# Kernel optimization log

Hardware: AMD Instinct MI355X
Metric: run time of the kernel (lower is better)

Reference implementation:

```python
import jax, jax.numpy as jnp
import numpy as np
import math

# ---- static config (must match init_kwargs / input_specs) ----
D = 1024
N_HEAD = 16
HEAD_DIM = D // N_HEAD          # 64
HALF = HEAD_DIM // 2            # rope half dim = 32
N_EXP = 8
TOP_K = 2
CAP_FACTOR = 2.0
LN_EPS = 1e-5


def _build_sin_cos(T, half_dim, dtype=jnp.float32):
    pos = jnp.arange(T, dtype=dtype)[:, None]                      # (T,1)
    inv_freq = 1.0 / (10000.0 ** (jnp.arange(0, 2 * half_dim, 2, dtype=dtype) / (2 * half_dim)))
    ang = pos * inv_freq[None, :]                                  # (T, half)
    return jnp.sin(ang), jnp.cos(ang)


def _layernorm(x, g, b):
    mu = jnp.mean(x, axis=-1, keepdims=True)
    var = jnp.mean(jnp.square(x - mu), axis=-1, keepdims=True)
    return (x - mu) * jax.lax.rsqrt(var + LN_EPS) * g + b


def _apply_rope(q, k, sin, cos):
    # q,k: (B,T,H,hd); sin,cos: (T, half)
    s = sin[None, :, None, :]
    c = cos[None, :, None, :]
    q1, q2 = q[..., :HALF], q[..., HALF:]
    k1, k2 = k[..., :HALF], k[..., HALF:]
    qr = jnp.concatenate([q1 * c - q2 * s, q1 * s + q2 * c], axis=-1)
    kr = jnp.concatenate([k1 * c - k2 * s, k1 * s + k2 * c], axis=-1)
    return qr, kr


def _attention(x, Wqkv, Wproj):
    B, T, C = x.shape
    qkv = x @ Wqkv                                                  # (B,T,3C)
    qkv = qkv.reshape(B, T, N_HEAD, 3 * HEAD_DIM)
    q, k, v = jnp.split(qkv, 3, axis=-1)                            # each (B,T,H,hd)
    sin, cos = _build_sin_cos(T, HALF)
    q, k = _apply_rope(q, k, sin, cos)
    scale = 1.0 / math.sqrt(HEAD_DIM)
    att = jnp.einsum('bqhd,bkhd->bhqk', q, k) * scale               # (B,H,T,T)
    causal = jnp.tril(jnp.ones((T, T), dtype=bool))
    att = jnp.where(causal[None, None], att, jnp.finfo(att.dtype).min)
    p = jax.nn.softmax(att, axis=-1)
    o = jnp.einsum('bhqk,bkhd->bqhd', p, v).reshape(B, T, C)
    return o @ Wproj, k, v


def _sparse_moe(flat, Wgate, W1, b1, W2, b2):
    # flat: (N, d). Eval mode: no router noise.
    N, d = flat.shape
    capacity = int(math.ceil(CAP_FACTOR * N / N_EXP))
    logits = flat @ Wgate                                           # (N,E)
    gates = jax.nn.softmax(logits, axis=-1)
    vals, inds = jax.lax.top_k(gates, TOP_K)                        # (N,k)
    flat_inds = inds.reshape(-1)                                    # (N*k,)
    flat_vals = vals.reshape(-1)
    neg = jnp.finfo(flat.dtype).min
    # per-expert assignment scores over all (token, slot) pairs
    scores = jnp.where(flat_inds[None, :] == jnp.arange(N_EXP)[:, None],
                       flat_vals[None, :], neg)                     # (E, N*k)
    top_scores, top_pos = jax.lax.top_k(scores, capacity)           # (E, cap)
    tok_idx = top_pos // TOP_K                                      # (E, cap)
    w = jnp.where(top_scores > neg, top_scores, 0.0)                # dropped slots -> 0 weight
    xe = flat[tok_idx]                                              # gather: (E, cap, d)
    h = jax.nn.gelu(jnp.einsum('ecd,edh->ech', xe, W1) + b1[:, None, :], approximate=False)
    out = jnp.einsum('ech,ehd->ecd', h, W2) + b2[:, None, :]
    out = out * w[..., None]
    final = jnp.zeros_like(flat).at[tok_idx.reshape(-1)].add(out.reshape(-1, d))
    return final


def setup_inputs() -> dict:
    key = jax.random.key(0)
    ks = jax.random.split(key, 10)
    B, T = 2, 2048
    s = 0.02
    return {
        'x': jax.random.normal(ks[0], (B, T, D), dtype=jnp.float32),
        'ln1_g': jnp.ones((D,), jnp.float32),
        'ln1_b': jnp.zeros((D,), jnp.float32),
        'ln2_g': jnp.ones((D,), jnp.float32),
        'ln2_b': jnp.zeros((D,), jnp.float32),
        'Wqkv': jax.random.normal(ks[1], (D, 3 * D), jnp.float32) * s,
        'Wproj': jax.random.normal(ks[2], (D, D), jnp.float32) * s,
        'Wgate': jax.random.normal(ks[3], (D, N_EXP), jnp.float32) * s,
        'W1': jax.random.normal(ks[4], (N_EXP, D, 4 * D), jnp.float32) * s,
        'b1': jnp.zeros((N_EXP, 4 * D), jnp.float32),
        'W2': jax.random.normal(ks[5], (N_EXP, 4 * D, D), jnp.float32) * s,
        'b2': jnp.zeros((N_EXP, D), jnp.float32),
    }


def reference(x, ln1_g, ln1_b, ln2_g, ln2_b, Wqkv, Wproj, Wgate, W1, b1, W2, b2):
    B, T, _ = x.shape
    x_norm = _layernorm(x, ln1_g, ln1_b)
    attn_out, k, v = _attention(x_norm, Wqkv, Wproj)
    x = x + attn_out
    ff_in = _layernorm(x, ln2_g, ln2_b)
    moe_out = _sparse_moe(ff_in.reshape(B * T, D), Wgate, W1, b1, W2, b2)
    x = x + moe_out.reshape(B, T, D)
    aux_loss = jnp.zeros((), x.dtype)  # eval mode
    return x, aux_loss, k, v
```

## Files before the change

kernel.cpp:

```cpp
#include <hip/hip_runtime.h>
#include <hip/hip_bf16.h>
#include <math.h>


#define TT 2048
#define NTOK 4096

typedef __attribute__((ext_vector_type(8))) short bf16x8;
typedef __attribute__((ext_vector_type(4))) float f32x4;
typedef __attribute__((ext_vector_type(16))) float f32x16;

static __device__ __forceinline__ ushort f2bf(float f) {
  union { float f; unsigned u; } v; v.f = f;
  unsigned r = v.u + 0x7FFFu + ((v.u >> 16) & 1u);
  return (ushort)(r >> 16);
}
static __device__ __forceinline__ float bf2f(ushort h) {
  union { unsigned u; float f; } v; v.u = ((unsigned)h) << 16; return v.f;
}
static __device__ __forceinline__ unsigned cvt_pk_bf16(float lo, float hi) {
  unsigned r;
  asm("v_cvt_pk_bf16_f32 %0, %1, %2" : "=v"(r) : "v"(lo), "v"(hi));
  return r;
}
static __device__ __forceinline__ void plane_swap(unsigned& a, unsigned& b) {
  asm("v_permlane32_swap_b32 %0, %1" : "+v"(a), "+v"(b));
}
static __device__ __forceinline__ void gload16(const void* g, void* l) {
  __builtin_amdgcn_global_load_lds(
      (const __attribute__((address_space(1))) void*)g,
      (__attribute__((address_space(3))) void*)l, 16, 0, 0);
}

template<bool WF32>
__global__ __launch_bounds__(256)
void ln_kernel(const float* __restrict__ x, const float* __restrict__ g,
               const float* __restrict__ b, float* __restrict__ out,
               ushort* __restrict__ oh, ushort* __restrict__ ol) {
  int row = blockIdx.x, tid = threadIdx.x;
  const float4* xr = (const float4*)(x + (size_t)row * 1024);
  float4 v = xr[tid];
  float s = v.x + v.y + v.z + v.w;
  #pragma unroll
  for (int off = 1; off < 64; off <<= 1) s += __shfl_xor(s, off);
  __shared__ float red1[4], red2[4];
  if ((tid & 63) == 0) red1[tid >> 6] = s;
  __syncthreads();
  float mu = (red1[0] + red1[1] + red1[2] + red1[3]) * (1.0f / 1024.0f);
  float dx = v.x - mu, dy = v.y - mu, dz = v.z - mu, dw = v.w - mu;
  float ss = dx*dx + dy*dy + dz*dz + dw*dw;
  #pragma unroll
  for (int off = 1; off < 64; off <<= 1) ss += __shfl_xor(ss, off);
  if ((tid & 63) == 0) red2[tid >> 6] = ss;
  __syncthreads();
  float var = (red2[0] + red2[1] + red2[2] + red2[3]) * (1.0f / 1024.0f);
  float inv = 1.0f / sqrtf(var + 1e-5f);
  float4 g4 = ((const float4*)g)[tid];
  float4 b4 = ((const float4*)b)[tid];
  float4 o4;
  o4.x = dx * inv * g4.x + b4.x;
  o4.y = dy * inv * g4.y + b4.y;
  o4.z = dz * inv * g4.z + b4.z;
  o4.w = dw * inv * g4.w + b4.w;
  if constexpr (WF32)
    ((float4*)(out + (size_t)row * 1024))[tid] = o4;
  size_t base = (size_t)row * 1024 + tid * 4;
  ushort h0 = f2bf(o4.x), h1 = f2bf(o4.y), h2 = f2bf(o4.z), h3 = f2bf(o4.w);
  ushort4 hh = {h0, h1, h2, h3};
  *(ushort4*)(oh + base) = hh;
  ushort4 ll = {f2bf(o4.x - bf2f(h0)), f2bf(o4.y - bf2f(h1)),
                f2bf(o4.z - bf2f(h2)), f2bf(o4.w - bf2f(h3))};
  *(ushort4*)(ol + base) = ll;
}

__global__ void sincos_kernel(float* __restrict__ st, float* __restrict__ ct) {
  int t = blockIdx.x, j = threadIdx.x;
  double invf = pow(10000.0, -((double)(2 * j)) / 64.0);
  double ang = (double)t * invf;
  st[t * 32 + j] = (float)sin(ang);
  ct[t * 32 + j] = (float)cos(ang);
}

__global__ __launch_bounds__(256)
void rope_kernel(float* __restrict__ qkv, const float* __restrict__ st,
                 const float* __restrict__ ct, float* __restrict__ kout,
                 float* __restrict__ vout, ushort* __restrict__ Kh,
                 ushort* __restrict__ Kl) {
  int row = blockIdx.x;
  int t = row & (TT - 1);
  int b = row >> 11;
  int tid = threadIdx.x;
  float* base = qkv + (size_t)row * 3072;
  #pragma unroll
  for (int l = 0; l < 2; ++l) {
    int idx = l * 256 + tid;
    int h = idx >> 5, j = idx & 31;
    float s = st[t * 32 + j], c = ct[t * 32 + j];
    float* qp = base + h * 192;
    float q1 = qp[j], q2 = qp[j + 32];
    qp[j]      = q1 * c - q2 * s;
    qp[j + 32] = q1 * s + q2 * c;
    float k1 = qp[64 + j], k2 = qp[96 + j];
    float kr1 = k1 * c - k2 * s, kr2 = k1 * s + k2 * c;
    qp[64 + j] = kr1; qp[96 + j] = kr2;
    kout[(size_t)row * 1024 + h * 64 + j]      = kr1;
    kout[(size_t)row * 1024 + h * 64 + 32 + j] = kr2;
    size_t kb = ((size_t)(b * 16 + h) * TT + t) * 64;
    ushort h1 = f2bf(kr1);
    Kh[kb + j] = h1; Kl[kb + j] = f2bf(kr1 - bf2f(h1));
    ushort h2 = f2bf(kr2);
    Kh[kb + 32 + j] = h2; Kl[kb + 32 + j] = f2bf(kr2 - bf2f(h2));
  }
  #pragma unroll
  for (int l = 0; l < 4; ++l) {
    int f = l * 256 + tid;
    int h = f >> 6, d = f & 63;
    vout[(size_t)row * 1024 + f] = base[h * 192 + 128 + d];
  }
}

__global__ __launch_bounds__(256)
void vtprep_kernel(const float* __restrict__ vout, ushort* __restrict__ Vth,
                   ushort* __restrict__ Vtl) {
  __shared__ float tile[64][65];
  int t0 = blockIdx.x * 64, h = blockIdx.y, b = blockIdx.z;
  int tid = threadIdx.x;
  #pragma unroll
  for (int l = 0; l < 4; ++l) {
    int idx = l * 256 + tid;
    int r = idx >> 4, c4 = (idx & 15) * 4;
    *(float4*)&tile[r][c4] = *(const float4*)&vout[((size_t)(b * TT + t0 + r)) * 1024 + h * 64 + c4];
  }
  __syncthreads();
  int d = tid >> 2, ts = (tid & 3) * 16;
  union { bf16x8 v; ushort u[8]; } H0, H1, L0, L1;
  #pragma unroll
  for (int i = 0; i < 8; ++i) {
    float v0 = tile[ts + i][d];
    ushort hb0 = f2bf(v0);
    H0.u[i] = hb0; L0.u[i] = f2bf(v0 - bf2f(hb0));
    float v1 = tile[ts + 8 + i][d];
    ushort hb1 = f2bf(v1);
    H1.u[i] = hb1; L1.u[i] = f2bf(v1 - bf2f(hb1));
  }
  size_t basep = ((size_t)(b * 16 + h) * 64 + d) * TT + t0 + ts;
  *(bf16x8*)(Vth + basep) = H0.v;  *(bf16x8*)(Vth + basep + 8) = H1.v;
  *(bf16x8*)(Vtl + basep) = L0.v;  *(bf16x8*)(Vtl + basep + 8) = L1.v;
}

__global__ __launch_bounds__(256)
void flash6_kernel(const float* __restrict__ qkv, const ushort* __restrict__ Kh,
                   const ushort* __restrict__ Kl, const ushort* __restrict__ Vth,
                   const ushort* __restrict__ Vtl, float* __restrict__ Opart,
                   float* __restrict__ Mpart, float* __restrict__ Lpart) {
  int lin = blockIdx.x;
  int xcd = lin & 7, s = lin >> 3;
  int bh = xcd + 8 * (s / 40);
  int j = 39 - (s % 40);
  int qt, kc;
  if (j < 4)       { qt = j;                    kc = 0; }
  else if (j < 12) { qt = 4 + ((j - 4) >> 1);   kc = (j - 4) & 1; }
  else if (j < 24) { qt = 8 + (j - 12) / 3;     kc = (j - 12) % 3; }
  else             { qt = 12 + ((j - 24) >> 2); kc = (j - 24) & 3; }
  int slot = bh * 40 + j;
  int h = bh & 15, b = bh >> 4;
  int tid = threadIdx.x;
  int w = tid >> 6, lane = tid & 63;
  int q = lane & 31, LH = lane >> 5;
  size_t bT = (size_t)b * TT;
  int qglob0 = qt * 128 + w * 32;
  int qg = qglob0 + q;
  bf16x8 qH[4], qL[4];
  {
    const float* qp = qkv + (bT + qg) * 3072 + h * 192 + LH * 8;
    #pragma unroll
    for (int dblk = 0; dblk < 4; ++dblk) {
      float4 f0 = *(const float4*)(qp + dblk * 16);
      float4 f1 = *(const float4*)(qp + dblk * 16 + 4);
      float vals[8] = {f0.x, f0.y, f0.z, f0.w, f1.x, f1.y, f1.z, f1.w};
      union { bf16x8 v; ushort u[8]; } H, L;
      #pragma unroll
      for (int e = 0; e < 8; ++e) {
        ushort hb = f2bf(vals[e]);
        H.u[e] = hb; L.u[e] = f2bf(vals[e] - bf2f(hb));
      }
      qH[dblk] = H.v; qL[dblk] = L.v;
    }
  }
  const ushort* Kbh = Kh + (size_t)bh * TT * 64;
  const ushort* Kbl = Kl + (size_t)bh * TT * 64;
  const ushort* Vbh = Vth + (size_t)bh * 64 * TT;
  const ushort* Vbl = Vtl + (size_t)bh * 64 * TT;
  f32x16 accO0 = {}, accO1 = {};
  float m = -3.402823466e38f, lsum = 0.0f;
  int kvlo = kc * 512;
  int kvhi = min(kc * 512 + 512, qglob0 + 32);

  for (int kv0 = kvlo; kv0 < kvhi; kv0 += 32) {
    const ushort* kbh = Kbh + (size_t)(kv0 + q) * 64 + LH * 8;
    const ushort* kbl = Kbl + (size_t)(kv0 + q) * 64 + LH * 8;
    bf16x8 kAH[4], kAL[4];
    #pragma unroll
    for (int dblk = 0; dblk < 4; ++dblk) {
      kAH[dblk] = *(const bf16x8*)(kbh + dblk * 16);
      kAL[dblk] = *(const bf16x8*)(kbl + dblk * 16);
    }
    f32x16 sa = {}, sb = {};
    sa = __builtin_amdgcn_mfma_f32_32x32x16_bf16(kAH[0], qH[0], sa, 0, 0, 0);
    sb = __builtin_amdgcn_mfma_f32_32x32x16_bf16(kAH[2], qH[2], sb, 0, 0, 0);
    sa = __builtin_amdgcn_mfma_f32_32x32x16_bf16(kAH[1], qH[1], sa, 0, 0, 0);
    sb = __builtin_amdgcn_mfma_f32_32x32x16_bf16(kAH[3], qH[3], sb, 0, 0, 0);
    sa = __builtin_amdgcn_mfma_f32_32x32x16_bf16(kAH[0], qL[0], sa, 0, 0, 0);
    sb = __builtin_amdgcn_mfma_f32_32x32x16_bf16(kAH[2], qL[2], sb, 0, 0, 0);
    sa = __builtin_amdgcn_mfma_f32_32x32x16_bf16(kAH[1], qL[1], sa, 0, 0, 0);
    sb = __builtin_amdgcn_mfma_f32_32x32x16_bf16(kAH[3], qL[3], sb, 0, 0, 0);
    sa = __builtin_amdgcn_mfma_f32_32x32x16_bf16(kAL[0], qH[0], sa, 0, 0, 0);
    sb = __builtin_amdgcn_mfma_f32_32x32x16_bf16(kAL[2], qH[2], sb, 0, 0, 0);
    sa = __builtin_amdgcn_mfma_f32_32x32x16_bf16(kAL[1], qH[1], sa, 0, 0, 0);
    sb = __builtin_amdgcn_mfma_f32_32x32x16_bf16(kAL[3], qH[3], sb, 0, 0, 0);
    bf16x8 vAH[2][2], vAL[2][2];
    #pragma unroll
    for (int dblk = 0; dblk < 2; ++dblk)
      #pragma unroll
      for (int s2 = 0; s2 < 2; ++s2) {
        size_t ad = (size_t)(dblk * 32 + q) * TT + kv0 + s2 * 16 + LH * 8;
        vAH[dblk][s2] = *(const bf16x8*)(Vbh + ad);
        vAL[dblk][s2] = *(const bf16x8*)(Vbl + ad);
      }
    float p[16];
    float pmax = -3.402823466e38f;
    if (kv0 + 31 > qglob0) {
      #pragma unroll
      for (int r = 0; r < 16; ++r) {
        int kvg = kv0 + (r & 3) + 8 * (r >> 2) + 4 * LH;
        float sv = (kvg <= qg) ? (sa[r] + sb[r]) * 0.125f : -3.402823466e38f;
        p[r] = sv; pmax = fmaxf(pmax, sv);
      }
    } else {
      #pragma unroll
      for (int r = 0; r < 16; ++r) {
        float sv = (sa[r] + sb[r]) * 0.125f;
        p[r] = sv; pmax = fmaxf(pmax, sv);
      }
    }
    pmax = fmaxf(pmax, __shfl_xor(pmax, 32));
    float mnew = fmaxf(m, pmax);
    float fsc = __expf(m - mnew);
    float psum = 0.0f;
    #pragma unroll
    for (int r = 0; r < 16; ++r) { p[r] = __expf(p[r] - mnew); psum += p[r]; }
    psum += __shfl_xor(psum, 32);
    lsum = lsum * fsc + psum;
    m = mnew;
    #pragma unroll
    for (int r = 0; r < 16; ++r) { accO0[r] *= fsc; accO1[r] *= fsc; }
    bf16x8 pHf[2], pLf[2];
    #pragma unroll
    for (int s2 = 0; s2 < 2; ++s2) {
      int s8 = s2 * 8;
      unsigned a  = cvt_pk_bf16(p[s8 + 0], p[s8 + 1]);
      unsigned bw = cvt_pk_bf16(p[s8 + 2], p[s8 + 3]);
      unsigned c  = cvt_pk_bf16(p[s8 + 4], p[s8 + 5]);
      unsigned d  = cvt_pk_bf16(p[s8 + 6], p[s8 + 7]);
      float l0 = p[s8 + 0] - __uint_as_float(a << 16);
      float l1 = p[s8 + 1] - __uint_as_float(a & 0xFFFF0000u);
      float l2 = p[s8 + 2] - __uint_as_float(bw << 16);
      float l3 = p[s8 + 3] - __uint_as_float(bw & 0xFFFF0000u);
      float l4 = p[s8 + 4] - __uint_as_float(c << 16);
      float l5 = p[s8 + 5] - __uint_as_float(c & 0xFFFF0000u);
      float l6 = p[s8 + 6] - __uint_as_float(d << 16);
      float l7 = p[s8 + 7] - __uint_as_float(d & 0xFFFF0000u);
      unsigned al = cvt_pk_bf16(l0, l1);
      unsigned bl = cvt_pk_bf16(l2, l3);
      unsigned cl = cvt_pk_bf16(l4, l5);
      unsigned dl = cvt_pk_bf16(l6, l7);
      plane_swap(a, c); plane_swap(bw, d);
      plane_swap(al, cl); plane_swap(bl, dl);
      union { unsigned w[4]; bf16x8 v; } PH, PL;
      PH.w[0] = a;  PH.w[1] = bw; PH.w[2] = c;  PH.w[3] = d;
      PL.w[0] = al; PL.w[1] = bl; PL.w[2] = cl; PL.w[3] = dl;
      pHf[s2] = PH.v; pLf[s2] = PL.v;
    }
    #pragma unroll
    for (int s2 = 0; s2 < 2; ++s2) {
      accO0 = __builtin_amdgcn_mfma_f32_32x32x16_bf16(vAH[0][s2], pHf[s2], accO0, 0, 0, 0);
      accO1 = __builtin_amdgcn_mfma_f32_32x32x16_bf16(vAH[1][s2], pHf[s2], accO1, 0, 0, 0);
      accO0 = __builtin_amdgcn_mfma_f32_32x32x16_bf16(vAH[0][s2], pLf[s2], accO0, 0, 0, 0);
      accO1 = __builtin_amdgcn_mfma_f32_32x32x16_bf16(vAH[1][s2], pLf[s2], accO1, 0, 0, 0);
      accO0 = __builtin_amdgcn_mfma_f32_32x32x16_bf16(vAL[0][s2], pHf[s2], accO0, 0, 0, 0);
      accO1 = __builtin_amdgcn_mfma_f32_32x32x16_bf16(vAL[1][s2], pHf[s2], accO1, 0, 0, 0);
    }
  }
  if (LH == 0) {
    Mpart[slot * 128 + w * 32 + q] = m;
    Lpart[slot * 128 + w * 32 + q] = lsum;
  }
  float* Ob = Opart + (size_t)slot * 8192 + (w * 32 + q) * 64;
  #pragma unroll
  for (int g2 = 0; g2 < 4; ++g2) {
    float4 v0 = {accO0[g2 * 4 + 0], accO0[g2 * 4 + 1], accO0[g2 * 4 + 2], accO0[g2 * 4 + 3]};
    *(float4*)(Ob + 8 * g2 + 4 * LH) = v0;
    float4 v1 = {accO1[g2 * 4 + 0], accO1[g2 * 4 + 1], accO1[g2 * 4 + 2], accO1[g2 * 4 + 3]};
    *(float4*)(Ob + 32 + 8 * g2 + 4 * LH) = v1;
  }
}

__global__ __launch_bounds__(256)
void fmerge2_kernel(const float* __restrict__ Opart, const float* __restrict__ Mpart,
                    const float* __restrict__ Lpart, ushort* __restrict__ oh,
                    ushort* __restrict__ ol) {
  int qt = blockIdx.x, bh = blockIdx.y;
  int h = bh & 15, b = bh >> 4;
  int g = qt >> 2;
  int nc = g + 1;
  int off = 2 * g * (g + 1) + (qt & 3) * (g + 1);
  int slot0 = bh * 40 + off;
  int tid = threadIdx.x;
  int q = tid & 127, dh = tid >> 7;
  float mg = -3.402823466e38f;
  for (int c = 0; c < nc; ++c) mg = fmaxf(mg, Mpart[(slot0 + c) * 128 + q]);
  float lg = 0.0f;
  float4 acc[8] = {};
  for (int c = 0; c < nc; ++c) {
    float sc = __expf(Mpart[(slot0 + c) * 128 + q] - mg);
    lg += sc * Lpart[(slot0 + c) * 128 + q];
    const float4* op = (const float4*)(Opart + (size_t)(slot0 + c) * 8192 + q * 64 + dh * 32);
    #pragma unroll
    for (int i = 0; i < 8; ++i) {
      float4 v = op[i];
      acc[i].x += sc * v.x; acc[i].y += sc * v.y;
      acc[i].z += sc * v.z; acc[i].w += sc * v.w;
    }
  }
  float inv = 1.0f / lg;
  size_t obase = ((size_t)(b * TT + qt * 128 + q)) * 1024 + h * 64 + dh * 32;
  #pragma unroll
  for (int i = 0; i < 8; ++i) {
    float4 v = {acc[i].x * inv, acc[i].y * inv, acc[i].z * inv, acc[i].w * inv};
    ushort h0 = f2bf(v.x), h1 = f2bf(v.y), h2 = f2bf(v.z), h3 = f2bf(v.w);
    ushort4 hh = {h0, h1, h2, h3};
    *(ushort4*)(oh + obase + i * 4) = hh;
    ushort4 ll = {f2bf(v.x - bf2f(h0)), f2bf(v.y - bf2f(h1)),
                  f2bf(v.z - bf2f(h2)), f2bf(v.w - bf2f(h3))};
    *(ushort4*)(ol + obase + i * 4) = ll;
  }
}

template<bool LO>
__global__ void tconv_kernel(const float* __restrict__ in, ushort* __restrict__ oh,
                             ushort* __restrict__ ol, int K, int N) {
  __shared__ float t[32][33];
  int z = blockIdx.z;
  const float* ip = in + (size_t)z * K * N;
  ushort* ohp = oh + (size_t)z * K * N;
  ushort* olp = LO ? (ol + (size_t)z * K * N) : nullptr;
  int n0 = blockIdx.x * 32, k0 = blockIdx.y * 32;
  int tx = threadIdx.x, ty = threadIdx.y;
  #pragma unroll
  for (int i = 0; i < 4; ++i)
    t[ty + 8 * i][tx] = ip[(size_t)(k0 + ty + 8 * i) * N + n0 + tx];
  __syncthreads();
  #pragma unroll
  for (int i = 0; i < 4; ++i) {
    float v = t[tx][ty + 8 * i];
    size_t off = (size_t)(n0 + ty + 8 * i) * K + k0 + tx;
    ushort hb = f2bf(v);
    ohp[off] = hb;
    if (LO) olp[off] = f2bf(v - bf2f(hb));
  }
}

template<int EPI, bool GATHER, bool SPLIT3>
__global__ __launch_bounds__(256, 2)
void mgemm(const ushort* __restrict__ Ah, const ushort* __restrict__ Al,
           const ushort* __restrict__ Bh, const ushort* __restrict__ Bl,
           void* __restrict__ Cv, const float* __restrict__ extra,
           const int* __restrict__ gatAll, int N, int K,
           long aEStride, long bEStride, long cEStride, int biasEStride) {
  __shared__ ushort As[128 * 64];
  __shared__ ushort Bs[128 * 64];
  int z = blockIdx.z;
  const ushort* AhB = Ah + (size_t)z * aEStride;
  const ushort* AlB = SPLIT3 ? (Al + (size_t)z * aEStride) : nullptr;
  const ushort* BhB = Bh + (size_t)z * bEStride;
  const ushort* BlB = SPLIT3 ? (Bl + (size_t)z * bEStride) : nullptr;
  const int* gat = GATHER ? (gatAll + z * 1024) : nullptr;
  int bm = blockIdx.y * 128, bn = blockIdx.x * 128;
  int tid = threadIdx.x;
  int wid = tid >> 6, lane = tid & 63;
  int w32 = wid * 32;
  int lrow = lane >> 3, cph = lane & 7;
  int garow[4];
  #pragma unroll
  for (int i = 0; i < 4; ++i) {
    int row = w32 + i * 8 + lrow;
    garow[i] = GATHER ? gat[bm + row] : (bm + row);
  }
  int kPer = K >> 6;
  int kSteps = (SPLIT3 ? 3 : 1) * kPer;
  int wm = wid >> 1, wn = wid & 1;
  int lr = lane & 15, lk = lane >> 4;
  f32x4 acc[4][4] = {};

  for (int t = 0; t < kSteps; ++t) {
    int seg = SPLIT3 ? (t / kPer) : 0;
    int kk = (SPLIT3 ? (t % kPer) : t) << 6;
    const ushort* Ause = (SPLIT3 && seg == 2) ? AlB : AhB;
    const ushort* Buse = (SPLIT3 && seg == 1) ? BlB : BhB;
    __syncthreads();
    #pragma unroll
    for (int i = 0; i < 4; ++i) {
      int row = w32 + i * 8 + lrow;
      int sc = cph ^ (row & 7);
      gload16(Ause + (size_t)garow[i] * K + kk + sc * 8, As + (w32 + i * 8) * 64);
      gload16(Buse + (size_t)(bn + row) * K + kk + sc * 8, Bs + (w32 + i * 8) * 64);
    }
    __syncthreads();
    #pragma unroll
    for (int kh = 0; kh < 2; ++kh) {
      bf16x8 af[4], bfr[4];
      #pragma unroll
      for (int mf = 0; mf < 4; ++mf) {
        int row = wm * 64 + mf * 16 + lr;
        int ch = (kh * 4 + lk) ^ (row & 7);
        af[mf] = *(const bf16x8*)&As[row * 64 + ch * 8];
      }
      #pragma unroll
      for (int nf = 0; nf < 4; ++nf) {
        int row = wn * 64 + nf * 16 + lr;
        int ch = (kh * 4 + lk) ^ (row & 7);
        bfr[nf] = *(const bf16x8*)&Bs[row * 64 + ch * 8];
      }
      #pragma unroll
      for (int mf = 0; mf < 4; ++mf)
        #pragma unroll
        for (int nf = 0; nf < 4; ++nf)
          acc[mf][nf] = __builtin_amdgcn_mfma_f32_16x16x32_bf16(af[mf], bfr[nf], acc[mf][nf], 0, 0, 0);
    }
  }
  int crow = bm + wm * 64, ccol = bn + wn * 64;
  if constexpr (EPI <= 1) {
    float* C = (float*)Cv;
    #pragma unroll
    for (int mf = 0; mf < 4; ++mf)
      #pragma unroll
      for (int nf = 0; nf < 4; ++nf)
        #pragma unroll
        for (int r = 0; r < 4; ++r) {
          int row = crow + mf * 16 + lk * 4 + r;
          int col = ccol + nf * 16 + lr;
          float v = acc[mf][nf][r];
          if constexpr (EPI == 1) v += extra[(size_t)row * N + col];
          C[(size_t)row * N + col] = v;
        }
  } else {
    const float* bias = extra + (size_t)z * biasEStride;
    ushort* C = (ushort*)Cv + (size_t)z * cEStride;
    #pragma unroll
    for (int mf = 0; mf < 4; ++mf)
      #pragma unroll
      for (int nf = 0; nf < 4; ++nf)
        #pragma unroll
        for (int r = 0; r < 4; ++r) {
          int row = crow + mf * 16 + lk * 4 + r;
          int col = ccol + nf * 16 + lr;
          float v = acc[mf][nf][r] + bias[col];
          if constexpr (EPI == 2)
            v = 0.5f * v * (1.0f + erff(v * 0.70710678118654752f));
          C[(size_t)row * N + col] = f2bf(v);
        }
  }
}

__global__ __launch_bounds__(256)
void gate_kernel(const float* __restrict__ ffin, const float* __restrict__ Wg,
                 int* __restrict__ te, float* __restrict__ tv, int* __restrict__ inv) {
  int token = blockIdx.x, tid = threadIdx.x;
  float acc[8] = {};
  const float* xr = ffin + (size_t)token * 1024;
  for (int i = tid; i < 1024; i += 256) {
    float xv = xr[i];
    const float4* wr = (const float4*)&Wg[i * 8];
    float4 w0 = wr[0], w1 = wr[1];
    acc[0] += xv * w0.x; acc[1] += xv * w0.y; acc[2] += xv * w0.z; acc[3] += xv * w0.w;
    acc[4] += xv * w1.x; acc[5] += xv * w1.y; acc[6] += xv * w1.z; acc[7] += xv * w1.w;
  }
  #pragma unroll
  for (int off = 1; off < 64; off <<= 1)
    #pragma unroll
    for (int q = 0; q < 8; ++q) acc[q] += __shfl_xor(acc[q], off);
  __shared__ float red[4][8];
  if ((tid & 63) == 0)
    #pragma unroll
    for (int q = 0; q < 8; ++q) red[tid >> 6][q] = acc[q];
  __syncthreads();
  if (tid == 0) {
    float g[8];
    #pragma unroll
    for (int q = 0; q < 8; ++q) g[q] = red[0][q] + red[1][q] + red[2][q] + red[3][q];
    float mx = g[0];
    #pragma unroll
    for (int q = 1; q < 8; ++q) mx = fmaxf(mx, g[q]);
    float sum = 0.0f;
    #pragma unroll
    for (int q = 0; q < 8; ++q) { g[q] = expf(g[q] - mx); sum += g[q]; }
    float inv_s = 1.0f / sum;
    #pragma unroll
    for (int q = 0; q < 8; ++q) g[q] *= inv_s;
    int e1 = 0; float v1 = g[0];
    for (int q = 1; q < 8; ++q) if (g[q] > v1) { v1 = g[q]; e1 = q; }
    int e2 = -1; float v2 = -1.0f;
    for (int q = 0; q < 8; ++q) { if (q == e1) continue; if (g[q] > v2) { v2 = g[q]; e2 = q; } }
    te[token * 2] = e1; te[token * 2 + 1] = e2;
    tv[token * 2] = v1; tv[token * 2 + 1] = v2;
    inv[token * 2] = -1; inv[token * 2 + 1] = -1;
  }
}

__global__ __launch_bounds__(1024)
void route_sort_kernel(const int* __restrict__ te, const float* __restrict__ tv,
                       int* __restrict__ etok, float* __restrict__ ew,
                       int* __restrict__ inv) {
  __shared__ unsigned long long sk[4096];
  __shared__ int wcnt[16];
  __shared__ int base;
  int e = blockIdx.x, tid = threadIdx.x;
  int lane = tid & 63, wv = tid >> 6;
  if (tid == 0) base = 0;
  __syncthreads();
  for (int c = 0; c < 8; ++c) {
    int s = c * 1024 + tid;
    bool sel = (te[s] == e);
    unsigned long long ball = __ballot(sel);
    int pre = __popcll(ball & ((1ull << lane) - 1ull));
    if (lane == 0) wcnt[wv] = __popcll(ball);
    __syncthreads();
    int woff = 0, tot = 0;
    #pragma unroll
    for (int i = 0; i < 16; ++i) {
      int cc = wcnt[i];
      if (i < wv) woff += cc;
      tot += cc;
    }
    if (sel) {
      unsigned vb = __float_as_uint(tv[s]);
      sk[base + woff + pre] =
          ((unsigned long long)vb << 32) | (unsigned)(0xFFFFFFFFu - (unsigned)s);
    }
    __syncthreads();
    if (tid == 0) base += tot;
    __syncthreads();
  }
  int n = base;
  if (n > 1024) {
    int P = (n <= 2048) ? 2048 : 4096;
    for (int i = n + tid; i < P; i += 1024) sk[i] = 0ull;
    __syncthreads();
    for (int k = 2; k <= P; k <<= 1)
      for (int j = k >> 1; j > 0; j >>= 1) {
        for (int t = tid; t < (P >> 1); t += 1024) {
          int i = ((t & ~(j - 1)) << 1) | (t & (j - 1));
          int p = i | j;
          unsigned long long a = sk[i], bq = sk[p];
          bool desc = ((i & k) == 0);
          if (desc ? (a < bq) : (a > bq)) { sk[i] = bq; sk[p] = a; }
        }
        __syncthreads();
      }
  }
  int cap = n < 1024 ? n : 1024;
  if (tid < cap) {
    unsigned long long key = sk[tid];
    unsigned slot = 0xFFFFFFFFu - (unsigned)(key & 0xFFFFFFFFull);
    etok[e * 1024 + tid] = (int)(slot >> 1);
    ew[e * 1024 + tid] = __uint_as_float((unsigned)(key >> 32));
    inv[slot] = e * 1024 + tid;
  } else {
    etok[e * 1024 + tid] = 0;
    ew[e * 1024 + tid] = 0.0f;
  }
}

__global__ __launch_bounds__(256)
void combine_kernel(const float* __restrict__ xres, const ushort* __restrict__ eo,
                    const int* __restrict__ inv, const float* __restrict__ ew,
                    float* __restrict__ outx, float* __restrict__ aux) {
  int token = blockIdx.x;
  int d = threadIdx.x * 4;
  float4 acc = *(const float4*)&xres[(size_t)token * 1024 + d];
  #pragma unroll
  for (int j = 0; j < 2; ++j) {
    int p = inv[token * 2 + j];
    if (p >= 0) {
      float w = ew[p];
      const ushort* ep = eo + (size_t)p * 1024 + d;
      acc.x += w * bf2f(ep[0]); acc.y += w * bf2f(ep[1]);
      acc.z += w * bf2f(ep[2]); acc.w += w * bf2f(ep[3]);
    }
  }
  *(float4*)&outx[(size_t)token * 1024 + d] = acc;
  if (token == 0 && threadIdx.x == 0) aux[0] = 0.0f;
}

extern "C" void kernel_launch(void* const* d_in, const int* in_sizes, int n_in,
                              void* d_out, int out_size, void* d_ws, size_t ws_size,
                              hipStream_t stream) {
  const float* x     = (const float*)d_in[0];
  const float* ln1g  = (const float*)d_in[1];
  const float* ln1b  = (const float*)d_in[2];
  const float* ln2g  = (const float*)d_in[3];
  const float* ln2b  = (const float*)d_in[4];
  const float* Wqkv  = (const float*)d_in[5];
  const float* Wproj = (const float*)d_in[6];
  const float* Wg    = (const float*)d_in[7];
  const float* W1    = (const float*)d_in[8];
  const float* b1    = (const float*)d_in[9];
  const float* W2    = (const float*)d_in[10];
  const float* b2    = (const float*)d_in[11];

  float* out_x   = (float*)d_out;
  float* out_aux = out_x + 4194304;
  float* out_k   = out_aux + 1;
  float* out_v   = out_k + 4194304;

  float* ws   = (float*)d_ws;
  float* A    = ws;
  float* qkvb = ws + 4194304;
  float* o    = ws + 16777216;
  float* st   = ws + 20971520;
  float* ct   = ws + 21037056;
  int*   te   = (int*)(ws + 21102592);
  float* tv   = ws + 21110784;
  int*   etok = (int*)(ws + 21118976);
  float* ew   = ws + 21127168;
  int*   inv  = (int*)(ws + 21135360);
  ushort* bfAh = (ushort*)(ws + 21143552);
  ushort* bfAl = (ushort*)(ws + 23240704);
  ushort* BqH  = (ushort*)(ws + 25337856);
  ushort* BqL  = (ushort*)(ws + 26910720);
  ushort* BpH  = (ushort*)(ws + 28483584);
  ushort* BpL  = (ushort*)(ws + 29007872);
  ushort* W1t  = (ushort*)(ws + 29532160);
  ushort* W2t  = (ushort*)(ws + 46309376);
  ushort* eo   = (ushort*)(ws + 63086592);
  ushort* hbuf = (ushort*)(ws + 4194304);
  ushort* Kh_  = bfAh;
  ushort* Kl_  = bfAl;
  ushort* Vth_ = eo;
  ushort* Vtl_ = eo + 4194304;
  float* Opart = ws + 29532160;
  float* Mpart = ws + 40017920;
  float* Lpart = ws + 40181760;

  tconv_kernel<true ><<<dim3(96, 32, 1),  dim3(32, 8), 0, stream>>>(Wqkv,  BqH, BqL, 1024, 3072);
  tconv_kernel<true ><<<dim3(32, 32, 1),  dim3(32, 8), 0, stream>>>(Wproj, BpH, BpL, 1024, 1024);
  sincos_kernel<<<TT, 32, 0, stream>>>(st, ct);

  ln_kernel<false><<<NTOK, 256, 0, stream>>>(x, ln1g, ln1b, nullptr, bfAh, bfAl);
  mgemm<0, false, true><<<dim3(24, 32, 1), 256, 0, stream>>>(
      bfAh, bfAl, BqH, BqL, qkvb, nullptr, nullptr, 3072, 1024, 0, 0, 0, 0);
  rope_kernel<<<NTOK, 256, 0, stream>>>(qkvb, st, ct, out_k, out_v, Kh_, Kl_);
  vtprep_kernel<<<dim3(32, 16, 2), 256, 0, stream>>>(out_v, Vth_, Vtl_);
  flash6_kernel<<<1280, 256, 0, stream>>>(qkvb, Kh_, Kl_, Vth_, Vtl_, Opart, Mpart, Lpart);
  fmerge2_kernel<<<dim3(16, 32), 256, 0, stream>>>(Opart, Mpart, Lpart, bfAh, bfAl);
  mgemm<1, false, true><<<dim3(8, 32, 1), 256, 0, stream>>>(
      bfAh, bfAl, BpH, BpL, A, x, nullptr, 1024, 1024, 0, 0, 0, 0);
  tconv_kernel<false><<<dim3(128, 32, 8), dim3(32, 8), 0, stream>>>(W1, W1t, nullptr, 1024, 4096);
  tconv_kernel<false><<<dim3(32, 128, 8), dim3(32, 8), 0, stream>>>(W2, W2t, nullptr, 4096, 1024);
  ln_kernel<true><<<NTOK, 256, 0, stream>>>(A, ln2g, ln2b, o, bfAh, bfAl);
  gate_kernel<<<NTOK, 256, 0, stream>>>(o, Wg, te, tv, inv);
  route_sort_kernel<<<8, 1024, 0, stream>>>(te, tv, etok, ew, inv);
  mgemm<2, true, false><<<dim3(32, 8, 8), 256, 0, stream>>>(
      bfAh, nullptr, W1t, nullptr, hbuf, b1, etok, 4096, 1024,
      0, 4096L * 1024, 1024L * 4096, 4096);
  mgemm<3, false, false><<<dim3(8, 8, 8), 256, 0, stream>>>(
      hbuf, nullptr, W2t, nullptr, eo, b2, nullptr, 1024, 4096,
      1024L * 4096, 1024L * 4096, 1024L * 1024, 1024);
  combine_kernel<<<NTOK, 256, 0, stream>>>(A, eo, inv, ew, out_x, out_aux);
}
```

Baseline: 711.5 us.

## Double-buffer GEMM LDS loads, prescale Q, and skip stable softmax rescales

The MoE/projection GEMM now uses two LDS buffers and issues the global-to-LDS loads for the next K step before computing the current one, with one barrier per iteration instead of two. This is meant to hide load latency behind MFMA work, at the cost of doubling LDS use per block, which may lower occupancy. In attention, the 1/sqrt(d) scale is folded into Q at load time. The online-softmax max update and accumulator rescale are skipped when the new block max exceeds the running max by at most 8 across the wave, which trades a small bounded-overflow risk for fewer exp and multiply operations.

```diff
diff --git a/kernel.cpp b/kernel.cpp
--- a/kernel.cpp
+++ b/kernel.cpp
@@ -177,7 +177,8 @@
     for (int dblk = 0; dblk < 4; ++dblk) {
       float4 f0 = *(const float4*)(qp + dblk * 16);
       float4 f1 = *(const float4*)(qp + dblk * 16 + 4);
-      float vals[8] = {f0.x, f0.y, f0.z, f0.w, f1.x, f1.y, f1.z, f1.w};
+      float vals[8] = {f0.x * 0.125f, f0.y * 0.125f, f0.z * 0.125f, f0.w * 0.125f,
+                       f1.x * 0.125f, f1.y * 0.125f, f1.z * 0.125f, f1.w * 0.125f};
       union { bf16x8 v; ushort u[8]; } H, L;
       #pragma unroll
       for (int e = 0; e < 8; ++e) {
@@ -233,27 +234,30 @@
       #pragma unroll
       for (int r = 0; r < 16; ++r) {
         int kvg = kv0 + (r & 3) + 8 * (r >> 2) + 4 * LH;
-        float sv = (kvg <= qg) ? (sa[r] + sb[r]) * 0.125f : -3.402823466e38f;
+        float sv = (kvg <= qg) ? (sa[r] + sb[r]) : -3.402823466e38f;
         p[r] = sv; pmax = fmaxf(pmax, sv);
       }
     } else {
       #pragma unroll
       for (int r = 0; r < 16; ++r) {
-        float sv = (sa[r] + sb[r]) * 0.125f;
+        float sv = sa[r] + sb[r];
         p[r] = sv; pmax = fmaxf(pmax, sv);
       }
     }
     pmax = fmaxf(pmax, __shfl_xor(pmax, 32));
-    float mnew = fmaxf(m, pmax);
-    float fsc = __expf(m - mnew);
+    int stable = __all(pmax - m <= 8.0f);
+    float mnew = stable ? m : fmaxf(m, pmax);
+    float fsc = stable ? 1.0f : __expf(m - mnew);
     float psum = 0.0f;
     #pragma unroll
     for (int r = 0; r < 16; ++r) { p[r] = __expf(p[r] - mnew); psum += p[r]; }
     psum += __shfl_xor(psum, 32);
     lsum = lsum * fsc + psum;
     m = mnew;
-    #pragma unroll
-    for (int r = 0; r < 16; ++r) { accO0[r] *= fsc; accO1[r] *= fsc; }
+    if (!stable) {
+      #pragma unroll
+      for (int r = 0; r < 16; ++r) { accO0[r] *= fsc; accO1[r] *= fsc; }
+    }
     bf16x8 pHf[2], pLf[2];
     #pragma unroll
     for (int s2 = 0; s2 < 2; ++s2) {
@@ -370,6 +374,22 @@
   }
 }
 
+#define STAGE(buf, tt) do {                                                    \
+    int seg = SPLIT3 ? ((tt) / kPer) : 0;                                      \
+    int kk = (SPLIT3 ? ((tt) % kPer) : (tt)) << 6;                             \
+    const ushort* Ause = (SPLIT3 && seg == 2) ? AlB : AhB;                     \
+    const ushort* Buse = (SPLIT3 && seg == 1) ? BlB : BhB;                     \
+    _Pragma("unroll")                                                          \
+    for (int i = 0; i < 4; ++i) {                                              \
+      int row = w32 + i * 8 + lrow;                                            \
+      int sc = cph ^ (row & 7);                                                \
+      gload16(Ause + (size_t)garow[i] * K + kk + sc * 8,                       \
+              &As[buf][(w32 + i * 8) * 64]);                                   \
+      gload16(Buse + (size_t)(bn + row) * K + kk + sc * 8,                     \
+              &Bs[buf][(w32 + i * 8) * 64]);                                   \
+    }                                                                          \
+  } while (0)
+
 template<int EPI, bool GATHER, bool SPLIT3>
 __global__ __launch_bounds__(256, 2)
 void mgemm(const ushort* __restrict__ Ah, const ushort* __restrict__ Al,
@@ -377,8 +397,8 @@
            void* __restrict__ Cv, const float* __restrict__ extra,
            const int* __restrict__ gatAll, int N, int K,
            long aEStride, long bEStride, long cEStride, int biasEStride) {
-  __shared__ ushort As[128 * 64];
-  __shared__ ushort Bs[128 * 64];
+  __shared__ ushort As[2][128 * 64];
+  __shared__ ushort Bs[2][128 * 64];
   int z = blockIdx.z;
   const ushort* AhB = Ah + (size_t)z * aEStride;
   const ushort* AlB = SPLIT3 ? (Al + (size_t)z * aEStride) : nullptr;
@@ -402,20 +422,12 @@
   int lr = lane & 15, lk = lane >> 4;
   f32x4 acc[4][4] = {};
 
+  STAGE(0, 0);
+  asm volatile("s_waitcnt vmcnt(0)" ::: "memory");
+  __builtin_amdgcn_s_barrier();
   for (int t = 0; t < kSteps; ++t) {
-    int seg = SPLIT3 ? (t / kPer) : 0;
-    int kk = (SPLIT3 ? (t % kPer) : t) << 6;
-    const ushort* Ause = (SPLIT3 && seg == 2) ? AlB : AhB;
-    const ushort* Buse = (SPLIT3 && seg == 1) ? BlB : BhB;
-    __syncthreads();
-    #pragma unroll
-    for (int i = 0; i < 4; ++i) {
-      int row = w32 + i * 8 + lrow;
-      int sc = cph ^ (row & 7);
-      gload16(Ause + (size_t)garow[i] * K + kk + sc * 8, As + (w32 + i * 8) * 64);
-      gload16(Buse + (size_t)(bn + row) * K + kk + sc * 8, Bs + (w32 + i * 8) * 64);
-    }
-    __syncthreads();
+    int cur = t & 1;
+    if (t + 1 < kSteps) STAGE(cur ^ 1, t + 1);
     #pragma unroll
     for (int kh = 0; kh < 2; ++kh) {
       bf16x8 af[4], bfr[4];
@@ -423,13 +435,13 @@
       for (int mf = 0; mf < 4; ++mf) {
         int row = wm * 64 + mf * 16 + lr;
         int ch = (kh * 4 + lk) ^ (row & 7);
-        af[mf] = *(const bf16x8*)&As[row * 64 + ch * 8];
+        af[mf] = *(const bf16x8*)&As[cur][row * 64 + ch * 8];
       }
       #pragma unroll
       for (int nf = 0; nf < 4; ++nf) {
         int row = wn * 64 + nf * 16 + lr;
         int ch = (kh * 4 + lk) ^ (row & 7);
-        bfr[nf] = *(const bf16x8*)&Bs[row * 64 + ch * 8];
+        bfr[nf] = *(const bf16x8*)&Bs[cur][row * 64 + ch * 8];
       }
       #pragma unroll
       for (int mf = 0; mf < 4; ++mf)
@@ -437,6 +449,8 @@
         for (int nf = 0; nf < 4; ++nf)
           acc[mf][nf] = __builtin_amdgcn_mfma_f32_16x16x32_bf16(af[mf], bfr[nf], acc[mf][nf], 0, 0, 0);
     }
+    asm volatile("s_waitcnt vmcnt(0)" ::: "memory");
+    __builtin_amdgcn_s_barrier();
   }
   int crow = bm + wm * 64, ccol = bn + wn * 64;
   if constexpr (EPI <= 1) {
```

After: 767.9 us. 7.9% more time.
